# Kernel tuning notes

Hardware: AMD Instinct MI355X
Metric: run time of the kernel (lower is better)

The kernel has to match this reference:

```python
import jax, jax.numpy as jnp
import numpy as np

FP8_MAX = 448.0  # e4m3fn saturation value

def q8(x):
    """Round-to-nearest-even quantization to float8 e4m3fn values (kept in fp32).
    Normal min exponent -6, mantissa 3 bits, subnormal step 2^-9, saturate at 448."""
    a = jnp.abs(x)
    e = jnp.clip(jnp.floor(jnp.log2(jnp.maximum(a, 1e-30))), -6.0, 8.0)
    step = jnp.exp2(e - 3.0)  # mantissa quantization step for this binade
    q = jnp.minimum(jnp.round(a / step) * step, FP8_MAX)  # jnp.round is half-to-even
    return jnp.sign(x) * q

def setup_inputs() -> dict:
    key = jax.random.key(0)
    k1, k2, k3 = jax.random.split(key, 3)
    B, D_IN, D_H, D_OUT = 8192, 1024, 4096, 1024
    x = jax.random.normal(k1, (B, D_IN), jnp.float32)
    # learned weights (torch Linear layout: [out, in]); scaled to a realistic FP8 range
    w1 = jax.random.normal(k2, (D_H, D_IN), jnp.float32) * 0.03
    w2 = jax.random.normal(k3, (D_OUT, D_H), jnp.float32) * 0.03
    return {"x": x, "w1": w1, "w2": w2}

def reference(x, w1, w2):
    # x -> fp8 e4m3fn -> bit-pulse encode (lossless round trip for fp8 values)
    x8 = q8(x)
    # spike FP8 linear layers carry fp8 weights (set_weight_from_float quantizes)
    w1q = q8(w1)
    w2q = q8(w2)
    # fc1: spike spatial-encoding adder == accumulate wide, emit FP8 pulses
    h = q8(jnp.einsum('bi,hi->bh', x8, w1q))
    # SpikeFP8ReLU: zero out negative fp8 pulse values
    h = jnp.where(h > 0, h, 0.0)
    # fc2 then fp8_bits_to_float decode
    out = q8(jnp.einsum('bh,oh->bo', h, w2q))
    return out
```

## Files before the change

### kernel.cpp

```cpp
#include <hip/hip_runtime.h>
#include <stdint.h>
#include <stddef.h>

typedef int v4i  __attribute__((ext_vector_type(4)));
typedef int v16i __attribute__((ext_vector_type(16)));

#define KCH  512
#define PSTR 1040
#define BUFB (64 * PSTR)
#define LDSB (2 * BUFB)

__device__ __forceinline__ void gl_lds16(const uint8_t* g, uint8_t* l) {
    __builtin_amdgcn_global_load_lds(
        (const __attribute__((address_space(1))) uint32_t*)g,
        (__attribute__((address_space(3))) uint32_t*)l,
        16, 0, 0);
}

__device__ __forceinline__ float q8f(float v) {
    float a = fabsf(v);
    int e = (int)(__float_as_uint(a) >> 23) - 127;
    e = e < -6 ? -6 : (e > 8 ? 8 : e);
    float step  = __uint_as_float((uint32_t)(e - 3 + 127) << 23);
    float rstep = __uint_as_float((uint32_t)(3 - e + 127) << 23);
    float q = fminf(rintf(a * rstep) * step, 448.0f);
    return v < 0.0f ? -q : q;
}
__device__ __forceinline__ int qm(float v) {
    return (int)rintf(q8f(v) * 512.0f);
}

__device__ __forceinline__ uint32_t rne_sh(uint32_t a, int s) {
    uint32_t t = a >> s;
    uint32_t rem = a & ((1u << s) - 1u);
    uint32_t half = 1u << (s - 1);
    t += (rem > half) || (rem == half && (t & 1u));
    return t;
}

__global__ __launch_bounds__(256) void quant_x_kernel(
    const float* __restrict__ in, uint32_t* __restrict__ xh, uint32_t* __restrict__ xl, int n4) {
    int i = blockIdx.x * 256 + threadIdx.x;
    if (i >= n4) return;
    float4 v = ((const float4*)in)[i];
    int m0 = qm(v.x), m1 = qm(v.y), m2 = qm(v.z), m3 = qm(v.w);
    xh[i] = ((uint32_t)((m0 >> 5) & 0xff)) | ((uint32_t)((m1 >> 5) & 0xff) << 8) |
            ((uint32_t)((m2 >> 5) & 0xff) << 16) | ((uint32_t)((m3 >> 5) & 0xff) << 24);
    xl[i] = ((uint32_t)(m0 & 31)) | ((uint32_t)(m1 & 31) << 8) |
            ((uint32_t)(m2 & 31) << 16) | ((uint32_t)(m3 & 31) << 24);
}

__global__ __launch_bounds__(256) void quant_w_kernel(
    const float* __restrict__ in, uint32_t* __restrict__ wm, int n4) {
    int i = blockIdx.x * 256 + threadIdx.x;
    if (i >= n4) return;
    float4 v = ((const float4*)in)[i];
    wm[i] = ((uint32_t)(qm(v.x) & 0xff)) | ((uint32_t)(qm(v.y) & 0xff) << 8) |
            ((uint32_t)(qm(v.z) & 0xff) << 16) | ((uint32_t)(qm(v.w) & 0xff) << 24);
}

template <int EPI>
__global__ __launch_bounds__(512, 2) void gemm_i8_big(
    const uint8_t* __restrict__ Ah, const uint8_t* __restrict__ Al,
    const uint8_t* __restrict__ Bm,
    void* __restrict__ Ch, void* __restrict__ Cl,
    int M, int N, int K) {
    extern __shared__ uint8_t sB[];

    const int tid  = threadIdx.x;
    const int lane = tid & 63;
    const int wave = tid >> 6;
    const int col  = lane & 31;
    const int kh   = lane >> 5;
    const int bm = blockIdx.x, bn = blockIdx.y;

    v16i acc[2][4];
#pragma unroll
    for (int p = 0; p < 2; ++p)
#pragma unroll
        for (int j = 0; j < 4; ++j) acc[p][j] = (v16i)0;

    const size_t arow = (size_t)(bm * 256 + wave * 32 + col);
    const uint8_t* pAh = Ah + arow * K + kh * 16;
    const uint8_t* pAl = Al + arow * K + kh * 16;

    const size_t brow = (size_t)(bn * 128 + wave * 16 + kh);
    int bbase[4];
#pragma unroll
    for (int j = 0; j < 4; ++j)
        bbase[j] = (j * 16 + (col >> 1)) * PSTR + (col & 1) * 512 + kh * 16;

    const int NC = K / KCH;
    {
        const uint8_t* g = Bm + brow * K + (lane & 31) * 16;
        uint8_t* l = sB + wave * 8 * PSTR + lane * 16;
#pragma unroll
        for (int c = 0; c < 8; ++c)
            gl_lds16(g + (size_t)(2 * c) * K, l + c * PSTR);
    }

    for (int c = 0; c < NC; ++c) {
        __syncthreads();
        if (c + 1 < NC) {
            const uint8_t* g = Bm + brow * K + (c + 1) * KCH + (lane & 31) * 16;
            uint8_t* l = sB + ((c + 1) & 1) * BUFB + wave * 8 * PSTR + lane * 16;
#pragma unroll
            for (int s = 0; s < 8; ++s)
                gl_lds16(g + (size_t)(2 * s) * K, l + s * PSTR);
        }
        const uint8_t* bufc = sB + (c & 1) * BUFB;
        const int kc = c * KCH;
#pragma unroll 4
        for (int k0 = 0; k0 < KCH; k0 += 32) {
            v4i a0 = *(const v4i*)(pAh + kc + k0);
            v4i a1 = *(const v4i*)(pAl + kc + k0);
            v4i b[4];
#pragma unroll
            for (int j = 0; j < 4; ++j)
                b[j] = *(const v4i*)(bufc + bbase[j] + k0);
#pragma unroll
            for (int j = 0; j < 4; ++j) {
                acc[0][j] = __builtin_amdgcn_mfma_i32_32x32x32_i8(a0, b[j], acc[0][j], 0, 0, 0);
                acc[1][j] = __builtin_amdgcn_mfma_i32_32x32x32_i8(a1, b[j], acc[1][j], 0, 0, 0);
            }
        }
    }

    const int cg0 = bn * 128 + col;
    const int rg0 = bm * 256 + wave * 32 + 4 * kh;
#pragma unroll
    for (int j = 0; j < 4; ++j) {
#pragma unroll
        for (int reg = 0; reg < 16; ++reg) {
            int mt = acc[0][j][reg] * 32 + acc[1][j][reg];
            size_t idx = (size_t)(rg0 + (reg & 3) + 8 * (reg >> 2)) * N
                       + (size_t)(cg0 + j * 32);
            if (EPI == 0) {
                uint8_t hb = 0, lb = 0;
                if (mt > 0) {
                    int s = 28 - __builtin_clz((uint32_t)mt);
                    if (s < 9) s = 9;
                    int mh = (int)(rne_sh((uint32_t)mt, s) << (s - 9));
                    hb = (uint8_t)(mh >> 5);
                    lb = (uint8_t)(mh & 31);
                }
                ((uint8_t*)Ch)[idx] = hb;
                ((uint8_t*)Cl)[idx] = lb;
            } else {
                uint32_t a = mt < 0 ? (uint32_t)(-mt) : (uint32_t)mt;
                float v = 0.0f;
                if (a) {
                    int s = 28 - __builtin_clz(a);
                    if (s < 9) s = 9;
                    v = (float)(rne_sh(a, s) << s) * 0x1p-18f;
                    if (mt < 0) v = -v;
                }
                ((float*)Ch)[idx] = v;
            }
        }
    }
}

extern "C" void kernel_launch(void* const* d_in, const int* in_sizes, int n_in,
                              void* d_out, int out_size, void* d_ws, size_t ws_size,
                              hipStream_t stream) {
    const int Bsz = 8192, DIN = 1024, DH = 4096, DOUT = 1024;
    const float* x  = (const float*)d_in[0];
    const float* w1 = (const float*)d_in[1];
    const float* w2 = (const float*)d_in[2];
    float* out = (float*)d_out;

    uint8_t* ws  = (uint8_t*)d_ws;
    uint8_t* xh  = ws;
    uint8_t* xl  = xh  + (size_t)Bsz * DIN;
    uint8_t* w1m = xl  + (size_t)Bsz * DIN;
    uint8_t* w2m = w1m + (size_t)DH  * DIN;
    uint8_t* hh  = w2m + (size_t)DOUT * DH;
    uint8_t* hl  = hh  + (size_t)Bsz * DH;

    static bool attr_done = false;
    if (!attr_done) {
        hipFuncSetAttribute((const void*)gemm_i8_big<0>,
                            hipFuncAttributeMaxDynamicSharedMemorySize, LDSB);
        hipFuncSetAttribute((const void*)gemm_i8_big<1>,
                            hipFuncAttributeMaxDynamicSharedMemorySize, LDSB);
        attr_done = true;
    }

    quant_x_kernel<<<(Bsz * DIN / 4) / 256, 256, 0, stream>>>(
        x, (uint32_t*)xh, (uint32_t*)xl, Bsz * DIN / 4);
    quant_w_kernel<<<(DH * DIN / 4) / 256, 256, 0, stream>>>(
        w1, (uint32_t*)w1m, DH * DIN / 4);
    quant_w_kernel<<<(DOUT * DH / 4) / 256, 256, 0, stream>>>(
        w2, (uint32_t*)w2m, DOUT * DH / 4);

    dim3 g1(Bsz / 256, DH / 128);
    gemm_i8_big<0><<<g1, 512, LDSB, stream>>>(xh, xl, w1m, (void*)hh, (void*)hl, Bsz, DH, DIN);

    dim3 g2(Bsz / 256, DOUT / 128);
    gemm_i8_big<1><<<g2, 512, LDSB, stream>>>(hh, hl, w2m, (void*)out, nullptr, Bsz, DOUT, DH);
}
```

Before: 293.2 us.

## Shrink GEMM tile to 128x128, repack B LDS layout, fuse quant kernels

Merges the three quantization kernels into one launch to cut launch overhead. The int8 GEMM moves from 512-thread blocks with 256-row tiles to 256-thread blocks with 128-row tiles, and halves the K chunk to 256. The B tile in LDS is repacked from a padded row-stride layout into 16-byte K-granule slabs. The smaller tile doubles the grid for more blocks in flight and cuts LDS use, at the cost of more B reloads per output row.

```diff
diff --git a/kernel.cpp b/kernel.cpp
--- a/kernel.cpp
+++ b/kernel.cpp
@@ -5,9 +5,9 @@
 typedef int v4i  __attribute__((ext_vector_type(4)));
 typedef int v16i __attribute__((ext_vector_type(16)));
 
-#define KCH  512
-#define PSTR 1040
-#define BUFB (64 * PSTR)
+#define KCH  256
+#define GRAN (KCH / 16)
+#define BUFB (GRAN * 128 * 16)
 #define LDSB (2 * BUFB)
 
 __device__ __forceinline__ void gl_lds16(const uint8_t* g, uint8_t* l) {
@@ -38,29 +38,34 @@
     return t;
 }
 
-__global__ __launch_bounds__(256) void quant_x_kernel(
-    const float* __restrict__ in, uint32_t* __restrict__ xh, uint32_t* __restrict__ xl, int n4) {
+__global__ __launch_bounds__(256) void quant_all_kernel(
+    const float* __restrict__ x,  uint32_t* __restrict__ xh, uint32_t* __restrict__ xl,
+    const float* __restrict__ w1, uint32_t* __restrict__ w1m,
+    const float* __restrict__ w2, uint32_t* __restrict__ w2m,
+    int n4x, int n4w1, int n4w2) {
     int i = blockIdx.x * 256 + threadIdx.x;
-    if (i >= n4) return;
-    float4 v = ((const float4*)in)[i];
-    int m0 = qm(v.x), m1 = qm(v.y), m2 = qm(v.z), m3 = qm(v.w);
-    xh[i] = ((uint32_t)((m0 >> 5) & 0xff)) | ((uint32_t)((m1 >> 5) & 0xff) << 8) |
-            ((uint32_t)((m2 >> 5) & 0xff) << 16) | ((uint32_t)((m3 >> 5) & 0xff) << 24);
-    xl[i] = ((uint32_t)(m0 & 31)) | ((uint32_t)(m1 & 31) << 8) |
-            ((uint32_t)(m2 & 31) << 16) | ((uint32_t)(m3 & 31) << 24);
-}
-
-__global__ __launch_bounds__(256) void quant_w_kernel(
-    const float* __restrict__ in, uint32_t* __restrict__ wm, int n4) {
-    int i = blockIdx.x * 256 + threadIdx.x;
-    if (i >= n4) return;
-    float4 v = ((const float4*)in)[i];
-    wm[i] = ((uint32_t)(qm(v.x) & 0xff)) | ((uint32_t)(qm(v.y) & 0xff) << 8) |
-            ((uint32_t)(qm(v.z) & 0xff) << 16) | ((uint32_t)(qm(v.w) & 0xff) << 24);
+    if (i < n4x) {
+        float4 v = ((const float4*)x)[i];
+        int m0 = qm(v.x), m1 = qm(v.y), m2 = qm(v.z), m3 = qm(v.w);
+        xh[i] = ((uint32_t)((m0 >> 5) & 0xff)) | ((uint32_t)((m1 >> 5) & 0xff) << 8) |
+                ((uint32_t)((m2 >> 5) & 0xff) << 16) | ((uint32_t)((m3 >> 5) & 0xff) << 24);
+        xl[i] = ((uint32_t)(m0 & 31)) | ((uint32_t)(m1 & 31) << 8) |
+                ((uint32_t)(m2 & 31) << 16) | ((uint32_t)(m3 & 31) << 24);
+    } else if (i < n4x + n4w1) {
+        int j = i - n4x;
+        float4 v = ((const float4*)w1)[j];
+        w1m[j] = ((uint32_t)(qm(v.x) & 0xff)) | ((uint32_t)(qm(v.y) & 0xff) << 8) |
+                 ((uint32_t)(qm(v.z) & 0xff) << 16) | ((uint32_t)(qm(v.w) & 0xff) << 24);
+    } else if (i < n4x + n4w1 + n4w2) {
+        int j = i - n4x - n4w1;
+        float4 v = ((const float4*)w2)[j];
+        w2m[j] = ((uint32_t)(qm(v.x) & 0xff)) | ((uint32_t)(qm(v.y) & 0xff) << 8) |
+                 ((uint32_t)(qm(v.z) & 0xff) << 16) | ((uint32_t)(qm(v.w) & 0xff) << 24);
+    }
 }
 
 template <int EPI>
-__global__ __launch_bounds__(512, 2) void gemm_i8_big(
+__global__ __launch_bounds__(256, 2) void gemm_i8_big(
     const uint8_t* __restrict__ Ah, const uint8_t* __restrict__ Al,
     const uint8_t* __restrict__ Bm,
     void* __restrict__ Ch, void* __restrict__ Cl,
@@ -80,33 +85,35 @@
 #pragma unroll
         for (int j = 0; j < 4; ++j) acc[p][j] = (v16i)0;
 
-    const size_t arow = (size_t)(bm * 256 + wave * 32 + col);
+    const size_t arow = (size_t)(bm * 128 + wave * 32 + col);
     const uint8_t* pAh = Ah + arow * K + kh * 16;
     const uint8_t* pAl = Al + arow * K + kh * 16;
 
-    const size_t brow = (size_t)(bn * 128 + wave * 16 + kh);
-    int bbase[4];
-#pragma unroll
-    for (int j = 0; j < 4; ++j)
-        bbase[j] = (j * 16 + (col >> 1)) * PSTR + (col & 1) * 512 + kh * 16;
+    const int bboff = kh * 2048 + col * 16;
 
     const int NC = K / KCH;
     {
-        const uint8_t* g = Bm + brow * K + (lane & 31) * 16;
-        uint8_t* l = sB + wave * 8 * PSTR + lane * 16;
-#pragma unroll
-        for (int c = 0; c < 8; ++c)
-            gl_lds16(g + (size_t)(2 * c) * K, l + c * PSTR);
+        const int t0 = wave * 8;
+#pragma unroll
+        for (int s = 0; s < 8; ++s) {
+            const int t = t0 + s, g = t >> 1, rh = t & 1;
+            gl_lds16(Bm + (size_t)(bn * 128 + rh * 64 + lane) * K + g * 16,
+                     sB + g * 2048 + rh * 1024 + lane * 16);
+        }
     }
 
     for (int c = 0; c < NC; ++c) {
         __syncthreads();
         if (c + 1 < NC) {
-            const uint8_t* g = Bm + brow * K + (c + 1) * KCH + (lane & 31) * 16;
-            uint8_t* l = sB + ((c + 1) & 1) * BUFB + wave * 8 * PSTR + lane * 16;
-#pragma unroll
-            for (int s = 0; s < 8; ++s)
-                gl_lds16(g + (size_t)(2 * s) * K, l + s * PSTR);
+            const int kcn = (c + 1) * KCH;
+            uint8_t* dst = sB + ((c + 1) & 1) * BUFB;
+            const int t0 = wave * 8;
+#pragma unroll
+            for (int s = 0; s < 8; ++s) {
+                const int t = t0 + s, g = t >> 1, rh = t & 1;
+                gl_lds16(Bm + (size_t)(bn * 128 + rh * 64 + lane) * K + kcn + g * 16,
+                         dst + g * 2048 + rh * 1024 + lane * 16);
+            }
         }
         const uint8_t* bufc = sB + (c & 1) * BUFB;
         const int kc = c * KCH;
@@ -114,10 +121,11 @@
         for (int k0 = 0; k0 < KCH; k0 += 32) {
             v4i a0 = *(const v4i*)(pAh + kc + k0);
             v4i a1 = *(const v4i*)(pAl + kc + k0);
+            const uint8_t* bg = bufc + (k0 >> 4) * 2048 + bboff;
             v4i b[4];
 #pragma unroll
             for (int j = 0; j < 4; ++j)
-                b[j] = *(const v4i*)(bufc + bbase[j] + k0);
+                b[j] = *(const v4i*)(bg + j * 512);
 #pragma unroll
             for (int j = 0; j < 4; ++j) {
                 acc[0][j] = __builtin_amdgcn_mfma_i32_32x32x32_i8(a0, b[j], acc[0][j], 0, 0, 0);
@@ -127,7 +135,7 @@
     }
 
     const int cg0 = bn * 128 + col;
-    const int rg0 = bm * 256 + wave * 32 + 4 * kh;
+    const int rg0 = bm * 128 + wave * 32 + 4 * kh;
 #pragma unroll
     for (int j = 0; j < 4; ++j) {
 #pragma unroll
@@ -187,16 +195,14 @@
         attr_done = true;
     }
 
-    quant_x_kernel<<<(Bsz * DIN / 4) / 256, 256, 0, stream>>>(
-        x, (uint32_t*)xh, (uint32_t*)xl, Bsz * DIN / 4);
-    quant_w_kernel<<<(DH * DIN / 4) / 256, 256, 0, stream>>>(
-        w1, (uint32_t*)w1m, DH * DIN / 4);
-    quant_w_kernel<<<(DOUT * DH / 4) / 256, 256, 0, stream>>>(
-        w2, (uint32_t*)w2m, DOUT * DH / 4);
-
-    dim3 g1(Bsz / 256, DH / 128);
-    gemm_i8_big<0><<<g1, 512, LDSB, stream>>>(xh, xl, w1m, (void*)hh, (void*)hl, Bsz, DH, DIN);
-
-    dim3 g2(Bsz / 256, DOUT / 128);
-    gemm_i8_big<1><<<g2, 512, LDSB, stream>>>(hh, hl, w2m, (void*)out, nullptr, Bsz, DOUT, DH);
-}
+    const int n4x = Bsz * DIN / 4, n4w1 = DH * DIN / 4, n4w2 = DOUT * DH / 4;
+    quant_all_kernel<<<(n4x + n4w1 + n4w2) / 256, 256, 0, stream>>>(
+        x, (uint32_t*)xh, (uint32_t*)xl, w1, (uint32_t*)w1m, w2, (uint32_t*)w2m,
+        n4x, n4w1, n4w2);
+
+    dim3 g1(Bsz / 128, DH / 128);
+    gemm_i8_big<0><<<g1, 256, LDSB, stream>>>(xh, xl, w1m, (void*)hh, (void*)hl, Bsz, DH, DIN);
+
+    dim3 g2(Bsz / 128, DOUT / 128);
+    gemm_i8_big<1><<<g2, 256, LDSB, stream>>>(hh, hl, w2m, (void*)out, nullptr, Bsz, DOUT, DH);
+}
```

Measured after the change: 319.3 us. 1.09x slower.
